# Performance work log

Hardware: AMD Instinct MI355X
Metric: run time of the kernel (lower is better)

## Reference

```python
import jax, jax.numpy as jnp
import numpy as np
from jax.ops import segment_sum, segment_max

N_NODES = 50000
N_GRAPHS = 64
EPS = 1e-16


def gat_layer(x, src, dst, W, a_src, a_dst, b, n_nodes):
    # PyG GATConv, heads=1: shared linear, additive attention, per-dst softmax
    h = x @ W                                  # [N, H]
    al_s = h @ a_src                           # [N]
    al_d = h @ a_dst                           # [N]
    e = jax.nn.leaky_relu(al_s[src] + al_d[dst], 0.2)   # [E]
    # numerically stable segment softmax over edges grouped by dst
    m = segment_max(e, dst, num_segments=n_nodes)
    m = jnp.where(jnp.isfinite(m), m, 0.0)
    ex = jnp.exp(e - m[dst])
    denom = segment_sum(ex, dst, num_segments=n_nodes)
    alpha = ex / (denom[dst] + EPS)            # [E]
    out = segment_sum(alpha[:, None] * h[src], dst, num_segments=n_nodes)
    return out + b


def setup_inputs() -> dict:
    key = jax.random.key(0)
    ks = jax.random.split(key, 16)
    H = 128
    x = jax.random.normal(ks[0], (N_NODES, 4), dtype=jnp.float32)
    edge_index = jax.random.randint(ks[1], (2, 800000), 0, N_NODES, dtype=jnp.int64)
    batch = jnp.sort(jax.random.randint(ks[2], (N_NODES,), 0, N_GRAPHS, dtype=jnp.int64))

    def glorot(k, shape):
        lim = np.sqrt(6.0 / (shape[0] + shape[-1]))
        return jax.random.uniform(k, shape, jnp.float32, -lim, lim)

    params = {
        'W1': glorot(ks[3], (4, H)), 'as1': glorot(ks[4], (H,)), 'ad1': glorot(ks[5], (H,)), 'b1': jnp.zeros((H,), jnp.float32),
        'W2': glorot(ks[6], (H, H)), 'as2': glorot(ks[7], (H,)), 'ad2': glorot(ks[8], (H,)), 'b2': jnp.zeros((H,), jnp.float32),
        'W3': glorot(ks[9], (H, H)), 'as3': glorot(ks[10], (H,)), 'ad3': glorot(ks[11], (H,)), 'b3': jnp.zeros((H,), jnp.float32),
        'Wlin': glorot(ks[12], (H, 2)), 'blin': jnp.zeros((2,), jnp.float32),
    }
    return {'x': x, 'edge_index': edge_index, 'batch': batch, **params}


def reference(x, edge_index, batch, W1, as1, ad1, b1, W2, as2, ad2, b2, W3, as3, ad3, b3, Wlin, blin):
    n = x.shape[0]
    # GATConv default add_self_loops=True
    loop = jnp.arange(n, dtype=edge_index.dtype)
    src = jnp.concatenate([edge_index[0], loop])
    dst = jnp.concatenate([edge_index[1], loop])

    h = jax.nn.relu(gat_layer(x, src, dst, W1, as1, ad1, b1, n))
    h = jax.nn.relu(gat_layer(h, src, dst, W2, as2, ad2, b2, n))
    h = gat_layer(h, src, dst, W3, as3, ad3, b3, n)

    # global_mean_pool
    sums = segment_sum(h, batch, num_segments=N_GRAPHS)          # [G, H]
    cnt = segment_sum(jnp.ones((n,), h.dtype), batch, num_segments=N_GRAPHS)
    pooled = sums / jnp.maximum(cnt, 1.0)[:, None]
    # dropout p=0.5 is identity in eval mode
    return pooled @ Wlin + blin                                   # [G, 2]
```

## Files before the change

kernel.cpp:

```cpp
#include <hip/hip_runtime.h>
#include <math.h>


#define BW 512
#define PART_CHUNK 4096
#define HIST_WGS 256

typedef __attribute__((ext_vector_type(8))) short short8v;
typedef __attribute__((ext_vector_type(4))) float f32x4;
typedef __attribute__((ext_vector_type(4))) unsigned uint4v;

__device__ __forceinline__ float bflo(unsigned u) { return __uint_as_float(u << 16); }
__device__ __forceinline__ float bfhi(unsigned u) { return __uint_as_float(u & 0xffff0000u); }
__device__ __forceinline__ unsigned pk2bf(float a, float b) {
  unsigned ua = __float_as_uint(a); ua += 0x7fffu + ((ua >> 16) & 1u);
  unsigned ub = __float_as_uint(b); ub += 0x7fffu + ((ub >> 16) & 1u);
  return (ua >> 16) | (ub & 0xffff0000u);
}

__global__ __launch_bounds__(256) void kb_hist(const int* __restrict__ ei,
                                               int* __restrict__ bpart,
                                               int E, int ET) {
  __shared__ int h[128];
  int tid = threadIdx.x;
  if (tid < 128) h[tid] = 0;
  __syncthreads();
  int stride = HIST_WGS * 256;
  for (int i = blockIdx.x * 256 + tid; i < ET; i += stride) {
    int dst = (i < E) ? ei[E + i] : (i - E);
    atomicAdd(&h[dst >> 9], 1);
  }
  __syncthreads();
  if (tid < 128) bpart[blockIdx.x * 128 + tid] = h[tid];
}

__global__ __launch_bounds__(128) void kb_scan(const int* __restrict__ bpart,
                                               int* __restrict__ bbase,
                                               int* __restrict__ bcur,
                                               int* __restrict__ rowp,
                                               int N, int ET, int NB) {
  __shared__ int sm[128];
  int t = threadIdx.x;
  int v = 0;
  for (int w = 0; w < HIST_WGS; ++w) v += bpart[w * 128 + t];
  if (t >= NB) v = 0;
  sm[t] = v;
  __syncthreads();
  for (int off = 1; off < 128; off <<= 1) {
    int u = (t >= off) ? sm[t - off] : 0;
    __syncthreads();
    sm[t] += u;
    __syncthreads();
  }
  int pre = sm[t] - v;
  if (t <= NB) bbase[t] = pre;
  if (t < NB) bcur[t] = pre;
  if (t == 0) rowp[N] = ET;
}

__global__ __launch_bounds__(256) void kb_part(const int* __restrict__ ei,
                                               int* __restrict__ bcur,
                                               int* __restrict__ bucketed,
                                               int E, int ET, int NB) {
  __shared__ int hist[128];
  __shared__ int runb[128];
  int tid = threadIdx.x;
  int base = blockIdx.x * PART_CHUNK;
  if (tid < 128) hist[tid] = 0;

  int sv[16], dv[16];
#pragma unroll
  for (int k = 0; k < 16; ++k) {
    int j = base + k * 256 + tid;
    int s = -1, d = 0;
    if (j < ET) {
      if (j < E) { s = ei[j]; d = ei[E + j]; }
      else       { s = j - E; d = j - E; }
    }
    sv[k] = s; dv[k] = d;
  }
  __syncthreads();
#pragma unroll
  for (int k = 0; k < 16; ++k)
    if (sv[k] >= 0) atomicAdd(&hist[dv[k] >> 9], 1);
  __syncthreads();
  if (tid < NB && hist[tid] > 0) runb[tid] = atomicAdd(&bcur[tid], hist[tid]);
  __syncthreads();
  if (tid < 128) hist[tid] = 0;
  __syncthreads();
#pragma unroll
  for (int k = 0; k < 16; ++k) {
    if (sv[k] >= 0) {
      int b = dv[k] >> 9;
      int off = atomicAdd(&hist[b], 1);
      bucketed[runb[b] + off] = (sv[k] << 9) | (dv[k] & (BW - 1));
    }
  }
}

__global__ __launch_bounds__(256) void kb_csr(const int* __restrict__ bucketed,
                                              const int* __restrict__ bbase,
                                              int* __restrict__ rowp,
                                              int* __restrict__ csr,
                                              int N) {
  __shared__ int h[512];
  __shared__ int sm[256];
  __shared__ int cur[512];
  int tid = threadIdx.x;
  int b = blockIdx.x;
  int cb = bbase[b], ce = bbase[b + 1];

  h[tid] = 0; h[tid + 256] = 0;
  __syncthreads();
  for (int j = cb + tid; j < ce; j += 256)
    atomicAdd(&h[bucketed[j] & (BW - 1)], 1);
  __syncthreads();
  int a0 = h[2 * tid], a1 = h[2 * tid + 1];
  int s = a0 + a1;
  sm[tid] = s;
  __syncthreads();
  for (int off = 1; off < 256; off <<= 1) {
    int u = (tid >= off) ? sm[tid - off] : 0;
    __syncthreads();
    sm[tid] += u;
    __syncthreads();
  }
  int pre = sm[tid] - s;
  cur[2 * tid] = pre;
  cur[2 * tid + 1] = pre + a0;
  __syncthreads();
  int node0 = b * BW;
  for (int local = tid; local < BW; local += 256) {
    int node = node0 + local;
    if (node < N) rowp[node] = cb + cur[local];
  }
  __syncthreads();
  for (int j = cb + tid; j < ce; j += 256) {
    int p = bucketed[j];
    int loc = p & (BW - 1);
    int pos = cb + atomicAdd(&cur[loc], 1);
    csr[pos] = (unsigned)p >> 9;
  }
}

__global__ __launch_bounds__(256) void k_prep(const float* __restrict__ W2,
                                              const float* __restrict__ W3,
                                              const float* __restrict__ W1,
                                              const float* __restrict__ as1,
                                              const float* __restrict__ ad1,
                                              unsigned short* __restrict__ Wcm2,
                                              unsigned short* __restrict__ Wcm3,
                                              float* __restrict__ wv,
                                              float* __restrict__ gsum) {
  if (blockIdx.x >= 65) {
    int idx = (blockIdx.x - 65) * 256 + threadIdx.x;
    if (idx < 64 * 128 + 64) gsum[idx] = 0.f;
    return;
  }
  if (blockIdx.x == 64) {
    int lane = threadIdx.x;
    if (lane >= 64) return;
    float2 a = *(const float2*)(as1 + lane * 2);
    float2 d = *(const float2*)(ad1 + lane * 2);
    float ps[4], pd[4];
#pragma unroll
    for (int k = 0; k < 4; ++k) {
      float2 w = *(const float2*)(W1 + k * 128 + lane * 2);
      ps[k] = w.x * a.x + w.y * a.y;
      pd[k] = w.x * d.x + w.y * d.y;
    }
    for (int off = 32; off; off >>= 1) {
#pragma unroll
      for (int k = 0; k < 4; ++k) {
        ps[k] += __shfl_xor(ps[k], off);
        pd[k] += __shfl_xor(pd[k], off);
      }
    }
    if (lane == 0) {
#pragma unroll
      for (int k = 0; k < 4; ++k) { wv[k] = ps[k]; wv[4 + k] = pd[k]; }
    }
    return;
  }
  int i = blockIdx.x * 256 + threadIdx.x;
  if (i < 16384) {
    int k = i >> 7, n = i & 127;
    unsigned u = __float_as_uint(W2[i]); u += 0x7fffu + ((u >> 16) & 1u);
    Wcm2[n * 128 + k] = (unsigned short)(u >> 16);
    unsigned v = __float_as_uint(W3[i]); v += 0x7fffu + ((v >> 16) & 1u);
    Wcm3[n * 128 + k] = (unsigned short)(v >> 16);
  }
}

__global__ __launch_bounds__(256) void k_aggx1(const int* __restrict__ csr_src,
                                               const int* __restrict__ rowp,
                                               const float* __restrict__ wv,
                                               const float* __restrict__ X,
                                               const float* __restrict__ W,
                                               const float* __restrict__ bias,
                                               float* __restrict__ exw,
                                               unsigned* __restrict__ Ybf, int N) {
  int wid = threadIdx.x >> 6, lane = threadIdx.x & 63;
  int dst = blockIdx.x * 4 + wid;
  if (dst >= N) return;
  int beg = rowp[dst], end = rowp[dst + 1];
  int deg = end - beg;
  float wvs0 = wv[0], wvs1 = wv[1], wvs2 = wv[2], wvs3 = wv[3];
  float4 xd = *(const float4*)(X + (size_t)dst * 4);
  float ald = xd.x * wv[4] + xd.y * wv[5] + xd.z * wv[6] + xd.w * wv[7];
  float4 acc = {0.f, 0.f, 0.f, 0.f};

  if (deg <= 64) {
    int srcv = 0;
    float e = -INFINITY;
    float4 xv = {0.f, 0.f, 0.f, 0.f};
    if (lane < deg) {
      srcv = csr_src[beg + lane];
      xv = *(const float4*)(X + (size_t)srcv * 4);
      float als = xv.x * wvs0 + xv.y * wvs1 + xv.z * wvs2 + xv.w * wvs3;
      e = als + ald;
      e = (e > 0.f) ? e : 0.2f * e;
    }
    float m = e;
    for (int off = 32; off; off >>= 1) m = fmaxf(m, __shfl_xor(m, off));
    float av = (lane < deg) ? __expf(e - m) : 0.f;
    float den = av;
    for (int off = 32; off; off >>= 1) den += __shfl_xor(den, off);
    av *= 1.0f / (den + 1e-16f);
    acc.x = av * xv.x; acc.y = av * xv.y; acc.z = av * xv.z; acc.w = av * xv.w;
  } else {
    float m = -INFINITY;
    for (int j = beg + lane; j < end; j += 64) {
      int s = csr_src[j];
      float4 xv = *(const float4*)(X + (size_t)s * 4);
      float e = xv.x * wvs0 + xv.y * wvs1 + xv.z * wvs2 + xv.w * wvs3 + ald;
      e = (e > 0.f) ? e : 0.2f * e;
      exw[j] = e;
      m = fmaxf(m, e);
    }
    for (int off = 32; off; off >>= 1) m = fmaxf(m, __shfl_xor(m, off));
    float den = 0.f;
    for (int j = beg + lane; j < end; j += 64) {
      float ex = __expf(exw[j] - m);
      exw[j] = ex;
      den += ex;
    }
    for (int off = 32; off; off >>= 1) den += __shfl_xor(den, off);
    float inv = 1.0f / (den + 1e-16f);
    for (int j = beg + lane; j < end; j += 64) {
      int s = csr_src[j];
      float w = exw[j] * inv;
      float4 xv = *(const float4*)(X + (size_t)s * 4);
      acc.x += w * xv.x; acc.y += w * xv.y; acc.z += w * xv.z; acc.w += w * xv.w;
    }
  }
  for (int off = 32; off; off >>= 1) {
    acc.x += __shfl_xor(acc.x, off);
    acc.y += __shfl_xor(acc.y, off);
    acc.z += __shfl_xor(acc.z, off);
    acc.w += __shfl_xor(acc.w, off);
  }
  int f = lane * 2;
  float2 w0 = *(const float2*)(W + f);
  float2 w1 = *(const float2*)(W + 128 + f);
  float2 w2 = *(const float2*)(W + 256 + f);
  float2 w3 = *(const float2*)(W + 384 + f);
  float2 bv = *(const float2*)(bias + f);
  float h0 = acc.x * w0.x + acc.y * w1.x + acc.z * w2.x + acc.w * w3.x + bv.x;
  float h1 = acc.x * w0.y + acc.y * w1.y + acc.z * w2.y + acc.w * w3.y + bv.y;
  h0 = fmaxf(h0, 0.f); h1 = fmaxf(h1, 0.f);
  __builtin_nontemporal_store(pk2bf(h0, h1), Ybf + (size_t)dst * 64 + lane);
}

__global__ __launch_bounds__(256) void k_gemm128mfma(
    const unsigned short* __restrict__ Xbf,
    const unsigned short* __restrict__ Wcm,
    const float* __restrict__ asv, const float* __restrict__ adv,
    unsigned* __restrict__ Hbf,
    float* __restrict__ al_s, float* __restrict__ al_d, int N) {
  int wid = threadIdx.x >> 6, lane = threadIdx.x & 63;
  int c = lane & 15, g = lane >> 4;
  int row0 = blockIdx.x * 64 + wid * 16;
  int arow = row0 + c;
  int arowc = (arow < N) ? arow : (N - 1);

  short8v a[4];
#pragma unroll
  for (int kt = 0; kt < 4; ++kt)
    a[kt] = *(const short8v*)(Xbf + (size_t)arowc * 128 + kt * 32 + g * 8);

  f32x4 acc[8];
#pragma unroll
  for (int f = 0; f < 8; ++f) acc[f] = (f32x4){0.f, 0.f, 0.f, 0.f};

#pragma unroll
  for (int f = 0; f < 8; ++f) {
    const unsigned short* wb = Wcm + (size_t)(f * 16 + c) * 128 + g * 8;
#pragma unroll
    for (int kt = 0; kt < 4; ++kt) {
      short8v b = *(const short8v*)(wb + kt * 32);
      acc[f] = __builtin_amdgcn_mfma_f32_16x16x32_bf16(a[kt], b, acc[f], 0, 0, 0);
    }
  }

  float ps[4] = {0.f, 0.f, 0.f, 0.f}, pd[4] = {0.f, 0.f, 0.f, 0.f};
#pragma unroll
  for (int f = 0; f < 8; ++f) {
    float as_c = asv[f * 16 + c], ad_c = adv[f * 16 + c];
#pragma unroll
    for (int j = 0; j < 4; ++j) { ps[j] += acc[f][j] * as_c; pd[j] += acc[f][j] * ad_c; }
  }
#pragma unroll
  for (int j = 0; j < 4; ++j) {
    for (int off = 1; off < 16; off <<= 1) {
      ps[j] += __shfl_xor(ps[j], off);
      pd[j] += __shfl_xor(pd[j], off);
    }
  }
  if (c == 0) {
#pragma unroll
    for (int j = 0; j < 4; ++j) {
      int r = row0 + g * 4 + j;
      if (r < N) { al_s[r] = ps[j]; al_d[r] = pd[j]; }
    }
  }

#pragma unroll
  for (int f = 0; f < 8; ++f) {
#pragma unroll
    for (int j = 0; j < 4; ++j) {
      float partner = __shfl_xor(acc[f][j], 1);
      int r = row0 + g * 4 + j;
      if (((lane & 1) == 0) && r < N)
        __builtin_nontemporal_store(pk2bf(acc[f][j], partner),
                                    Hbf + (size_t)r * 64 + f * 8 + (c >> 1));
    }
  }
}

__global__ __launch_bounds__(256) void k_agg(const int* __restrict__ csr_src,
                                             const int* __restrict__ rowp,
                                             const float* __restrict__ al_s,
                                             const float* __restrict__ al_d,
                                             const uint4* __restrict__ Hbf,
                                             const float* __restrict__ bias,
                                             float* __restrict__ exw,
                                             unsigned* __restrict__ Ybf,
                                             int N, int relu) {
  int wid = threadIdx.x >> 6, lane = threadIdx.x & 63;
  int dst = blockIdx.x * 4 + wid;
  if (dst >= N) return;
  int beg = rowp[dst], end = rowp[dst + 1];
  int deg = end - beg;
  float ald = al_d[dst];

  int q = lane >> 4;
  int l = lane & 15;
  float acc[8];
#pragma unroll
  for (int c = 0; c < 8; ++c) acc[c] = 0.f;

  if (deg <= 64) {
    int srcv = 0;
    float e = -INFINITY;
    if (lane < deg) {
      srcv = csr_src[beg + lane];
      e = al_s[srcv] + ald;
      e = (e > 0.f) ? e : 0.2f * e;
    }
    float m = e;
    for (int off = 32; off; off >>= 1) m = fmaxf(m, __shfl_xor(m, off));
    float av = (lane < deg) ? __expf(e - m) : 0.f;
    float den = av;
    for (int off = 32; off; off >>= 1) den += __shfl_xor(den, off);
    av *= 1.0f / (den + 1e-16f);

    int t = 0;
    for (; t + 16 <= deg; t += 16) {
      int s0 = __shfl(srcv, t + q);
      int s1 = __shfl(srcv, t + 4 + q);
      int s2 = __shfl(srcv, t + 8 + q);
      int s3 = __shfl(srcv, t + 12 + q);
      float w0 = __shfl(av, t + q);
      float w1 = __shfl(av, t + 4 + q);
      float w2 = __shfl(av, t + 8 + q);
      float w3 = __shfl(av, t + 12 + q);
      uint4 v0 = Hbf[(size_t)s0 * 16 + l];
      uint4 v1 = Hbf[(size_t)s1 * 16 + l];
      uint4 v2 = Hbf[(size_t)s2 * 16 + l];
      uint4 v3 = Hbf[(size_t)s3 * 16 + l];
      acc[0] += w0 * bflo(v0.x) + w1 * bflo(v1.x) + w2 * bflo(v2.x) + w3 * bflo(v3.x);
      acc[1] += w0 * bfhi(v0.x) + w1 * bfhi(v1.x) + w2 * bfhi(v2.x) + w3 * bfhi(v3.x);
      acc[2] += w0 * bflo(v0.y) + w1 * bflo(v1.y) + w2 * bflo(v2.y) + w3 * bflo(v3.y);
      acc[3] += w0 * bfhi(v0.y) + w1 * bfhi(v1.y) + w2 * bfhi(v2.y) + w3 * bfhi(v3.y);
      acc[4] += w0 * bflo(v0.z) + w1 * bflo(v1.z) + w2 * bflo(v2.z) + w3 * bflo(v3.z);
      acc[5] += w0 * bfhi(v0.z) + w1 * bfhi(v1.z) + w2 * bfhi(v2.z) + w3 * bfhi(v3.z);
      acc[6] += w0 * bflo(v0.w) + w1 * bflo(v1.w) + w2 * bflo(v2.w) + w3 * bflo(v3.w);
      acc[7] += w0 * bfhi(v0.w) + w1 * bfhi(v1.w) + w2 * bfhi(v2.w) + w3 * bfhi(v3.w);
    }
    if (t + 8 <= deg) {
      int sA = __shfl(srcv, t + q);
      int sB = __shfl(srcv, t + 4 + q);
      float wA = __shfl(av, t + q);
      float wB = __shfl(av, t + 4 + q);
      uint4 va = Hbf[(size_t)sA * 16 + l];
      uint4 vb = Hbf[(size_t)sB * 16 + l];
      acc[0] += wA * bflo(va.x) + wB * bflo(vb.x);
      acc[1] += wA * bfhi(va.x) + wB * bfhi(vb.x);
      acc[2] += wA * bflo(va.y) + wB * bflo(vb.y);
      acc[3] += wA * bfhi(va.y) + wB * bfhi(vb.y);
      acc[4] += wA * bflo(va.z) + wB * bflo(vb.z);
      acc[5] += wA * bfhi(va.z) + wB * bfhi(vb.z);
      acc[6] += wA * bflo(va.w) + wB * bflo(vb.w);
      acc[7] += wA * bfhi(va.w) + wB * bfhi(vb.w);
      t += 8;
    }
    if (t + 4 <= deg) {
      int sA = __shfl(srcv, t + q);
      float wA = __shfl(av, t + q);
      uint4 va = Hbf[(size_t)sA * 16 + l];
      acc[0] += wA * bflo(va.x); acc[1] += wA * bfhi(va.x);
      acc[2] += wA * bflo(va.y); acc[3] += wA * bfhi(va.y);
      acc[4] += wA * bflo(va.z); acc[5] += wA * bfhi(va.z);
      acc[6] += wA * bflo(va.w); acc[7] += wA * bfhi(va.w);
      t += 4;
    }
    {
      int sA = __shfl(srcv, t + q);
      float wA = __shfl(av, t + q);
      if (t + q < deg) {
        uint4 va = Hbf[(size_t)sA * 16 + l];
        acc[0] += wA * bflo(va.x); acc[1] += wA * bfhi(va.x);
        acc[2] += wA * bflo(va.y); acc[3] += wA * bfhi(va.y);
        acc[4] += wA * bflo(va.z); acc[5] += wA * bfhi(va.z);
        acc[6] += wA * bflo(va.w); acc[7] += wA * bfhi(va.w);
      }
    }
  } else {
    float m = -INFINITY;
    for (int j = beg + lane; j < end; j += 64) {
      float e = al_s[csr_src[j]] + ald;
      e = (e > 0.f) ? e : 0.2f * e;
      exw[j] = e;
      m = fmaxf(m, e);
    }
    for (int off = 32; off; off >>= 1) m = fmaxf(m, __shfl_xor(m, off));

    float den = 0.f;
    for (int j = beg + lane; j < end; j += 64) {
      float ex = __expf(exw[j] - m);
      exw[j] = ex;
      den += ex;
    }
    for (int off = 32; off; off >>= 1) den += __shfl_xor(den, off);
    float inv = 1.0f / (den + 1e-16f);

    for (int j = beg + q; j < end; j += 4) {
      int sA = csr_src[j];
      float wA = exw[j] * inv;
      uint4 va = Hbf[(size_t)sA * 16 + l];
      acc[0] += wA * bflo(va.x); acc[1] += wA * bfhi(va.x);
      acc[2] += wA * bflo(va.y); acc[3] += wA * bfhi(va.y);
      acc[4] += wA * bflo(va.z); acc[5] += wA * bfhi(va.z);
      acc[6] += wA * bflo(va.w); acc[7] += wA * bfhi(va.w);
    }
  }

#pragma unroll
  for (int c = 0; c < 8; ++c) {
    acc[c] += __shfl_xor(acc[c], 16);
    acc[c] += __shfl_xor(acc[c], 32);
  }
  if (q == 0) {
    float4 bv0 = *(const float4*)(bias + l * 8);
    float4 bv1 = *(const float4*)(bias + l * 8 + 4);
    float o0 = acc[0] + bv0.x, o1 = acc[1] + bv0.y, o2 = acc[2] + bv0.z, o3 = acc[3] + bv0.w;
    float o4 = acc[4] + bv1.x, o5 = acc[5] + bv1.y, o6 = acc[6] + bv1.z, o7 = acc[7] + bv1.w;
    if (relu) {
      o0 = fmaxf(o0, 0.f); o1 = fmaxf(o1, 0.f); o2 = fmaxf(o2, 0.f); o3 = fmaxf(o3, 0.f);
      o4 = fmaxf(o4, 0.f); o5 = fmaxf(o5, 0.f); o6 = fmaxf(o6, 0.f); o7 = fmaxf(o7, 0.f);
    }
    uint4v pb;
    pb.x = pk2bf(o0, o1); pb.y = pk2bf(o2, o3);
    pb.z = pk2bf(o4, o5); pb.w = pk2bf(o6, o7);
    __builtin_nontemporal_store(pb, (uint4v*)(Ybf + (size_t)dst * 64 + l * 4));
  }
}

__global__ __launch_bounds__(256) void k_pool(const unsigned* __restrict__ Ybf,
                                              const int* __restrict__ batch,
                                              float* __restrict__ gsum,
                                              float* __restrict__ gcnt,
                                              int N, int nwaves) {
  int gw = (blockIdx.x * 256 + threadIdx.x) >> 6;
  int lane = threadIdx.x & 63;
  int chunk = (N + nwaves - 1) / nwaves;
  int beg = gw * chunk;
  int end = beg + chunk; if (end > N) end = N;
  if (beg >= end) return;

  int curg = batch[beg];
  float2 acc = {0.f, 0.f};
  int cnt = 0;
  for (int n = beg; n < end; ++n) {
    int g = batch[n];
    if (g != curg) {
      atomicAdd(&gsum[curg * 128 + lane * 2], acc.x);
      atomicAdd(&gsum[curg * 128 + lane * 2 + 1], acc.y);
      if (lane == 0) atomicAdd(&gcnt[curg], (float)cnt);
      acc.x = 0.f; acc.y = 0.f; cnt = 0; curg = g;
    }
    unsigned u = Ybf[(size_t)n * 64 + lane];
    acc.x += bflo(u); acc.y += bfhi(u);
    ++cnt;
  }
  atomicAdd(&gsum[curg * 128 + lane * 2], acc.x);
  atomicAdd(&gsum[curg * 128 + lane * 2 + 1], acc.y);
  if (lane == 0) atomicAdd(&gcnt[curg], (float)cnt);
}

__global__ __launch_bounds__(128) void k_final(const float* __restrict__ gsum,
                                               const float* __restrict__ gcnt,
                                               const float* __restrict__ Wlin,
                                               const float* __restrict__ blin,
                                               float* __restrict__ out) {
  int t = threadIdx.x;
  int g = t >> 1, c = t & 1;
  float inv = 1.0f / fmaxf(gcnt[g], 1.0f);
  float acc = blin[c];
  for (int k = 0; k < 128; ++k) acc += gsum[g * 128 + k] * inv * Wlin[k * 2 + c];
  out[g * 2 + c] = acc;
}

extern "C" void kernel_launch(void* const* d_in, const int* in_sizes, int n_in,
                              void* d_out, int out_size, void* d_ws, size_t ws_size,
                              hipStream_t stream) {
  const float* x    = (const float*)d_in[0];
  const int*   ei   = (const int*)d_in[1];
  const int*   batch= (const int*)d_in[2];
  const float* W1   = (const float*)d_in[3];
  const float* as1  = (const float*)d_in[4];
  const float* ad1  = (const float*)d_in[5];
  const float* b1   = (const float*)d_in[6];
  const float* W2   = (const float*)d_in[7];
  const float* as2  = (const float*)d_in[8];
  const float* ad2  = (const float*)d_in[9];
  const float* b2   = (const float*)d_in[10];
  const float* W3   = (const float*)d_in[11];
  const float* as3  = (const float*)d_in[12];
  const float* ad3  = (const float*)d_in[13];
  const float* b3   = (const float*)d_in[14];
  const float* Wlin = (const float*)d_in[15];
  const float* blin = (const float*)d_in[16];

  int N = in_sizes[0] / 4;
  int E = in_sizes[1] / 2;
  int ET = E + N;
  int NB = (N + BW - 1) / BW;

  char* ws = (char*)d_ws;
  unsigned* bfA = (unsigned*)ws; ws += (size_t)N * 64 * 4;
  unsigned* bfB = (unsigned*)ws; ws += (size_t)N * 64 * 4;
  float* al_s = (float*)ws; ws += (size_t)N * 4;
  float* al_d = (float*)ws; ws += (size_t)N * 4;
  float* wv   = (float*)ws; ws += (size_t)64 * 4;
  float* gsum = (float*)ws; ws += (size_t)64 * 128 * 4;
  float* gcnt = (float*)ws; ws += (size_t)64 * 4;
  int* rowp   = (int*)ws;   ws += (size_t)(N + 1) * 4;
  int* csr    = (int*)ws;   ws += (size_t)ET * 4;
  float* exw  = (float*)ws; ws += (size_t)ET * 4;
  int* bucketed = (int*)ws; ws += (size_t)ET * 4;
  int* bpart  = (int*)ws;   ws += (size_t)HIST_WGS * 128 * 4;
  int* bbase  = (int*)ws;   ws += (size_t)132 * 4;
  int* bcur   = (int*)ws;   ws += (size_t)128 * 4;
  unsigned short* wcm2 = (unsigned short*)ws; ws += (size_t)128 * 128 * 2;
  unsigned short* wcm3 = (unsigned short*)ws; ws += (size_t)128 * 128 * 2;

  kb_hist<<<HIST_WGS, 256, 0, stream>>>(ei, bpart, E, ET);
  kb_scan<<<1, 128, 0, stream>>>(bpart, bbase, bcur, rowp, N, ET, NB);
  kb_part<<<(ET + PART_CHUNK - 1) / PART_CHUNK, 256, 0, stream>>>(ei, bcur, bucketed, E, ET, NB);
  kb_csr <<<NB, 256, 0, stream>>>(bucketed, bbase, rowp, csr, N);
  k_prep <<<98, 256, 0, stream>>>(W2, W3, W1, as1, ad1, wcm2, wcm3, wv, gsum);

  int nb4 = (N + 3) / 4;
  int nb64 = (N + 63) / 64;
  k_aggx1<<<nb4, 256, 0, stream>>>(csr, rowp, wv, x, W1, b1, exw, bfB, N);
  k_gemm128mfma<<<nb64, 256, 0, stream>>>((const unsigned short*)bfB, wcm2, as2, ad2, bfA, al_s, al_d, N);
  k_agg        <<<nb4, 256, 0, stream>>>(csr, rowp, al_s, al_d, (const uint4*)bfA, b2, exw, bfB, N, 1);
  k_gemm128mfma<<<nb64, 256, 0, stream>>>((const unsigned short*)bfB, wcm3, as3, ad3, bfA, al_s, al_d, N);
  k_agg        <<<nb4, 256, 0, stream>>>(csr, rowp, al_s, al_d, (const uint4*)bfA, b3, exw, bfB, N, 0);

  k_pool <<<256, 256, 0, stream>>>(bfB, batch, gsum, gcnt, N, 1024);
  k_final<<<1, 128, 0, stream>>>(gsum, gcnt, Wlin, blin, (float*)d_out);
}
```

Before: 312.5 us.

## Process two destination nodes per wavefront in aggregation kernels and merge CSR/prep launches

```diff
diff --git a/kernel.cpp b/kernel.cpp
--- a/kernel.cpp
+++ b/kernel.cpp
@@ -4,11 +4,12 @@
 
 #define BW 512
 #define PART_CHUNK 4096
-#define HIST_WGS 256
+#define HIST_WGS 64
 
 typedef __attribute__((ext_vector_type(8))) short short8v;
 typedef __attribute__((ext_vector_type(4))) float f32x4;
 typedef __attribute__((ext_vector_type(4))) unsigned uint4v;
+typedef __attribute__((ext_vector_type(2))) unsigned uint2v;
 
 __device__ __forceinline__ float bflo(unsigned u) { return __uint_as_float(u << 16); }
 __device__ __forceinline__ float bfhi(unsigned u) { return __uint_as_float(u & 0xffff0000u); }
@@ -98,15 +99,65 @@
   }
 }
 
-__global__ __launch_bounds__(256) void kb_csr(const int* __restrict__ bucketed,
-                                              const int* __restrict__ bbase,
-                                              int* __restrict__ rowp,
-                                              int* __restrict__ csr,
-                                              int N) {
+__global__ __launch_bounds__(256) void kb_csrprep(const int* __restrict__ bucketed,
+                                                  const int* __restrict__ bbase,
+                                                  int* __restrict__ rowp,
+                                                  int* __restrict__ csr,
+                                                  const float* __restrict__ W2,
+                                                  const float* __restrict__ W3,
+                                                  const float* __restrict__ W1,
+                                                  const float* __restrict__ as1,
+                                                  const float* __restrict__ ad1,
+                                                  unsigned short* __restrict__ Wcm2,
+                                                  unsigned short* __restrict__ Wcm3,
+                                                  float* __restrict__ wv,
+                                                  float* __restrict__ gsum,
+                                                  int N, int NB) {
+  int tid = threadIdx.x;
+  if ((int)blockIdx.x >= NB) {
+    int pb = blockIdx.x - NB;
+    if (pb >= 65) {
+      int idx = (pb - 65) * 256 + tid;
+      if (idx < 64 * 128 + 64) gsum[idx] = 0.f;
+      return;
+    }
+    if (pb == 64) {
+      if (tid >= 64) return;
+      float2 a = *(const float2*)(as1 + tid * 2);
+      float2 d = *(const float2*)(ad1 + tid * 2);
+      float ps[4], pd[4];
+#pragma unroll
+      for (int k = 0; k < 4; ++k) {
+        float2 w = *(const float2*)(W1 + k * 128 + tid * 2);
+        ps[k] = w.x * a.x + w.y * a.y;
+        pd[k] = w.x * d.x + w.y * d.y;
+      }
+      for (int off = 32; off; off >>= 1) {
+#pragma unroll
+        for (int k = 0; k < 4; ++k) {
+          ps[k] += __shfl_xor(ps[k], off);
+          pd[k] += __shfl_xor(pd[k], off);
+        }
+      }
+      if (tid == 0) {
+#pragma unroll
+        for (int k = 0; k < 4; ++k) { wv[k] = ps[k]; wv[4 + k] = pd[k]; }
+      }
+      return;
+    }
+    int i = pb * 256 + tid;
+    if (i < 16384) {
+      int k = i >> 7, n = i & 127;
+      unsigned u = __float_as_uint(W2[i]); u += 0x7fffu + ((u >> 16) & 1u);
+      Wcm2[n * 128 + k] = (unsigned short)(u >> 16);
+      unsigned v = __float_as_uint(W3[i]); v += 0x7fffu + ((v >> 16) & 1u);
+      Wcm3[n * 128 + k] = (unsigned short)(v >> 16);
+    }
+    return;
+  }
   __shared__ int h[512];
   __shared__ int sm[256];
   __shared__ int cur[512];
-  int tid = threadIdx.x;
   int b = blockIdx.x;
   int cb = bbase[b], ce = bbase[b + 1];
 
@@ -143,73 +194,96 @@
   }
 }
 
-__global__ __launch_bounds__(256) void k_prep(const float* __restrict__ W2,
-                                              const float* __restrict__ W3,
-                                              const float* __restrict__ W1,
-                                              const float* __restrict__ as1,
-                                              const float* __restrict__ ad1,
-                                              unsigned short* __restrict__ Wcm2,
-                                              unsigned short* __restrict__ Wcm3,
-                                              float* __restrict__ wv,
-                                              float* __restrict__ gsum) {
-  if (blockIdx.x >= 65) {
-    int idx = (blockIdx.x - 65) * 256 + threadIdx.x;
-    if (idx < 64 * 128 + 64) gsum[idx] = 0.f;
-    return;
-  }
-  if (blockIdx.x == 64) {
-    int lane = threadIdx.x;
-    if (lane >= 64) return;
-    float2 a = *(const float2*)(as1 + lane * 2);
-    float2 d = *(const float2*)(ad1 + lane * 2);
-    float ps[4], pd[4];
-#pragma unroll
-    for (int k = 0; k < 4; ++k) {
-      float2 w = *(const float2*)(W1 + k * 128 + lane * 2);
-      ps[k] = w.x * a.x + w.y * a.y;
-      pd[k] = w.x * d.x + w.y * d.y;
-    }
-    for (int off = 32; off; off >>= 1) {
-#pragma unroll
-      for (int k = 0; k < 4; ++k) {
-        ps[k] += __shfl_xor(ps[k], off);
-        pd[k] += __shfl_xor(pd[k], off);
-      }
-    }
-    if (lane == 0) {
-#pragma unroll
-      for (int k = 0; k < 4; ++k) { wv[k] = ps[k]; wv[4 + k] = pd[k]; }
-    }
-    return;
-  }
-  int i = blockIdx.x * 256 + threadIdx.x;
-  if (i < 16384) {
-    int k = i >> 7, n = i & 127;
-    unsigned u = __float_as_uint(W2[i]); u += 0x7fffu + ((u >> 16) & 1u);
-    Wcm2[n * 128 + k] = (unsigned short)(u >> 16);
-    unsigned v = __float_as_uint(W3[i]); v += 0x7fffu + ((v >> 16) & 1u);
-    Wcm3[n * 128 + k] = (unsigned short)(v >> 16);
-  }
-}
-
-__global__ __launch_bounds__(256) void k_aggx1(const int* __restrict__ csr_src,
-                                               const int* __restrict__ rowp,
-                                               const float* __restrict__ wv,
-                                               const float* __restrict__ X,
-                                               const float* __restrict__ W,
-                                               const float* __restrict__ bias,
-                                               float* __restrict__ exw,
-                                               unsigned* __restrict__ Ybf, int N) {
-  int wid = threadIdx.x >> 6, lane = threadIdx.x & 63;
-  int dst = blockIdx.x * 4 + wid;
-  if (dst >= N) return;
-  int beg = rowp[dst], end = rowp[dst + 1];
+__device__ __forceinline__ void agg_full64(int beg, int end, float ald, int dst,
+    const int* __restrict__ csr_src, const float* __restrict__ al_s,
+    const uint4* __restrict__ Hbf, const float* __restrict__ bias,
+    float* __restrict__ exw, unsigned* __restrict__ Ybf, int relu) {
+  int lane = threadIdx.x & 63;
   int deg = end - beg;
-  float wvs0 = wv[0], wvs1 = wv[1], wvs2 = wv[2], wvs3 = wv[3];
-  float4 xd = *(const float4*)(X + (size_t)dst * 4);
-  float ald = xd.x * wv[4] + xd.y * wv[5] + xd.z * wv[6] + xd.w * wv[7];
+  int q = lane >> 4, l = lane & 15;
+  float acc[8];
+#pragma unroll
+  for (int c = 0; c < 8; ++c) acc[c] = 0.f;
+
+  if (deg <= 64) {
+    int srcv = 0;
+    float e = -INFINITY;
+    if (lane < deg) {
+      srcv = csr_src[beg + lane];
+      e = al_s[srcv] + ald;
+      e = (e > 0.f) ? e : 0.2f * e;
+    }
+    float m = e;
+    for (int off = 32; off; off >>= 1) m = fmaxf(m, __shfl_xor(m, off));
+    float av = (lane < deg) ? __expf(e - m) : 0.f;
+    float den = av;
+    for (int off = 32; off; off >>= 1) den += __shfl_xor(den, off);
+    av *= 1.0f / (den + 1e-16f);
+    for (int t = 0; t < deg; t += 4) {
+      int sA = __shfl(srcv, t + q);
+      float wA = __shfl(av, t + q);
+      uint4 va = Hbf[(size_t)sA * 16 + l];
+      acc[0] += wA * bflo(va.x); acc[1] += wA * bfhi(va.x);
+      acc[2] += wA * bflo(va.y); acc[3] += wA * bfhi(va.y);
+      acc[4] += wA * bflo(va.z); acc[5] += wA * bfhi(va.z);
+      acc[6] += wA * bflo(va.w); acc[7] += wA * bfhi(va.w);
+    }
+  } else {
+    float m = -INFINITY;
+    for (int j = beg + lane; j < end; j += 64) {
+      float e = al_s[csr_src[j]] + ald;
+      e = (e > 0.f) ? e : 0.2f * e;
+      exw[j] = e;
+      m = fmaxf(m, e);
+    }
+    for (int off = 32; off; off >>= 1) m = fmaxf(m, __shfl_xor(m, off));
+    float den = 0.f;
+    for (int j = beg + lane; j < end; j += 64) {
+      float ex = __expf(exw[j] - m);
+      exw[j] = ex;
+      den += ex;
+    }
+    for (int off = 32; off; off >>= 1) den += __shfl_xor(den, off);
+    float inv = 1.0f / (den + 1e-16f);
+    for (int j = beg + q; j < end; j += 4) {
+      int sA = csr_src[j];
+      float wA = exw[j] * inv;
+      uint4 va = Hbf[(size_t)sA * 16 + l];
+      acc[0] += wA * bflo(va.x); acc[1] += wA * bfhi(va.x);
+      acc[2] += wA * bflo(va.y); acc[3] += wA * bfhi(va.y);
+      acc[4] += wA * bflo(va.z); acc[5] += wA * bfhi(va.z);
+      acc[6] += wA * bflo(va.w); acc[7] += wA * bfhi(va.w);
+    }
+  }
+#pragma unroll
+  for (int c = 0; c < 8; ++c) {
+    acc[c] += __shfl_xor(acc[c], 16);
+    acc[c] += __shfl_xor(acc[c], 32);
+  }
+  if (q == 0) {
+    float4 bv0 = *(const float4*)(bias + l * 8);
+    float4 bv1 = *(const float4*)(bias + l * 8 + 4);
+    float o0 = acc[0] + bv0.x, o1 = acc[1] + bv0.y, o2 = acc[2] + bv0.z, o3 = acc[3] + bv0.w;
+    float o4 = acc[4] + bv1.x, o5 = acc[5] + bv1.y, o6 = acc[6] + bv1.z, o7 = acc[7] + bv1.w;
+    if (relu) {
+      o0 = fmaxf(o0, 0.f); o1 = fmaxf(o1, 0.f); o2 = fmaxf(o2, 0.f); o3 = fmaxf(o3, 0.f);
+      o4 = fmaxf(o4, 0.f); o5 = fmaxf(o5, 0.f); o6 = fmaxf(o6, 0.f); o7 = fmaxf(o7, 0.f);
+    }
+    uint4v pb;
+    pb.x = pk2bf(o0, o1); pb.y = pk2bf(o2, o3);
+    pb.z = pk2bf(o4, o5); pb.w = pk2bf(o6, o7);
+    __builtin_nontemporal_store(pb, (uint4v*)(Ybf + (size_t)dst * 64 + l * 4));
+  }
+}
+
+__device__ __forceinline__ void aggx1_full64(int beg, int end, float ald, int dst,
+    const int* __restrict__ csr_src, const float* __restrict__ X,
+    float wvs0, float wvs1, float wvs2, float wvs3,
+    const float* __restrict__ W, const float* __restrict__ bias,
+    float* __restrict__ exw, unsigned* __restrict__ Ybf) {
+  int lane = threadIdx.x & 63;
+  int deg = end - beg;
   float4 acc = {0.f, 0.f, 0.f, 0.f};
-
   if (deg <= 64) {
     int srcv = 0;
     float e = -INFINITY;
@@ -217,8 +291,7 @@
     if (lane < deg) {
       srcv = csr_src[beg + lane];
       xv = *(const float4*)(X + (size_t)srcv * 4);
-      float als = xv.x * wvs0 + xv.y * wvs1 + xv.z * wvs2 + xv.w * wvs3;
-      e = als + ald;
+      e = xv.x * wvs0 + xv.y * wvs1 + xv.z * wvs2 + xv.w * wvs3 + ald;
       e = (e > 0.f) ? e : 0.2f * e;
     }
     float m = e;
@@ -272,6 +345,88 @@
   __builtin_nontemporal_store(pk2bf(h0, h1), Ybf + (size_t)dst * 64 + lane);
 }
 
+__global__ __launch_bounds__(256) void k_aggx1(const int* __restrict__ csr_src,
+                                               const int* __restrict__ rowp,
+                                               const float* __restrict__ wv,
+                                               const float* __restrict__ X,
+                                               const float* __restrict__ W,
+                                               const float* __restrict__ bias,
+                                               float* __restrict__ exw,
+                                               unsigned* __restrict__ Ybf, int N) {
+  int wid = threadIdx.x >> 6, lane = threadIdx.x & 63;
+  int half = lane >> 5, il = lane & 31;
+  int d0 = blockIdx.x * 8 + wid * 2;
+  if (d0 >= N) return;
+  float wvs0 = wv[0], wvs1 = wv[1], wvs2 = wv[2], wvs3 = wv[3];
+  float wvd0 = wv[4], wvd1 = wv[5], wvd2 = wv[6], wvd3 = wv[7];
+
+  int dst = d0 + half;
+  bool vdst = dst < N;
+  int beg = 0, end = 0;
+  if (vdst) { beg = rowp[dst]; end = rowp[dst + 1]; }
+  int deg = end - beg;
+  int mx = max(deg, __shfl_xor(deg, 32));
+
+  float ald = 0.f;
+  if (vdst) {
+    float4 xd = *(const float4*)(X + (size_t)dst * 4);
+    ald = xd.x * wvd0 + xd.y * wvd1 + xd.z * wvd2 + xd.w * wvd3;
+  }
+
+  if (mx <= 32) {
+    int srcv = 0;
+    float e = -INFINITY;
+    float4 xv = {0.f, 0.f, 0.f, 0.f};
+    if (il < deg) {
+      srcv = csr_src[beg + il];
+      xv = *(const float4*)(X + (size_t)srcv * 4);
+      float e0 = xv.x * wvs0 + xv.y * wvs1 + xv.z * wvs2 + xv.w * wvs3 + ald;
+      e = (e0 > 0.f) ? e0 : 0.2f * e0;
+    }
+    float m = e;
+    for (int off = 16; off; off >>= 1) m = fmaxf(m, __shfl_xor(m, off));
+    float av = (il < deg) ? __expf(e - m) : 0.f;
+    float den = av;
+    for (int off = 16; off; off >>= 1) den += __shfl_xor(den, off);
+    av *= 1.0f / (den + 1e-16f);
+    float4 acc;
+    acc.x = av * xv.x; acc.y = av * xv.y; acc.z = av * xv.z; acc.w = av * xv.w;
+    for (int off = 16; off; off >>= 1) {
+      acc.x += __shfl_xor(acc.x, off);
+      acc.y += __shfl_xor(acc.y, off);
+      acc.z += __shfl_xor(acc.z, off);
+      acc.w += __shfl_xor(acc.w, off);
+    }
+    int f = il * 4;
+    float4 w0 = *(const float4*)(W + f);
+    float4 w1 = *(const float4*)(W + 128 + f);
+    float4 w2 = *(const float4*)(W + 256 + f);
+    float4 w3 = *(const float4*)(W + 384 + f);
+    float4 bv = *(const float4*)(bias + f);
+    float h0 = acc.x * w0.x + acc.y * w1.x + acc.z * w2.x + acc.w * w3.x + bv.x;
+    float h1 = acc.x * w0.y + acc.y * w1.y + acc.z * w2.y + acc.w * w3.y + bv.y;
+    float h2 = acc.x * w0.z + acc.y * w1.z + acc.z * w2.z + acc.w * w3.z + bv.z;
+    float h3 = acc.x * w0.w + acc.y * w1.w + acc.z * w2.w + acc.w * w3.w + bv.w;
+    h0 = fmaxf(h0, 0.f); h1 = fmaxf(h1, 0.f);
+    h2 = fmaxf(h2, 0.f); h3 = fmaxf(h3, 0.f);
+    if (vdst) {
+      uint2v pb;
+      pb.x = pk2bf(h0, h1); pb.y = pk2bf(h2, h3);
+      __builtin_nontemporal_store(pb, (uint2v*)(Ybf + (size_t)dst * 64 + il * 2));
+    }
+  } else {
+    for (int k = 0; k < 2; ++k) {
+      int d = d0 + k;
+      if (d < N) {
+        int b = rowp[d], en = rowp[d + 1];
+        float4 xd = *(const float4*)(X + (size_t)d * 4);
+        float a2 = xd.x * wvd0 + xd.y * wvd1 + xd.z * wvd2 + xd.w * wvd3;
+        aggx1_full64(b, en, a2, d, csr_src, X, wvs0, wvs1, wvs2, wvs3, W, bias, exw, Ybf);
+      }
+    }
+  }
+}
+
 __global__ __launch_bounds__(256) void k_gemm128mfma(
     const unsigned short* __restrict__ Xbf,
     const unsigned short* __restrict__ Wcm,
@@ -348,43 +503,47 @@
                                              unsigned* __restrict__ Ybf,
                                              int N, int relu) {
   int wid = threadIdx.x >> 6, lane = threadIdx.x & 63;
-  int dst = blockIdx.x * 4 + wid;
-  if (dst >= N) return;
-  int beg = rowp[dst], end = rowp[dst + 1];
+  int half = lane >> 5, il = lane & 31;
+  int d0 = blockIdx.x * 8 + wid * 2;
+  if (d0 >= N) return;
+  int dst = d0 + half;
+  bool vdst = dst < N;
+  int beg = 0, end = 0;
+  if (vdst) { beg = rowp[dst]; end = rowp[dst + 1]; }
   int deg = end - beg;
-  float ald = al_d[dst];
-
-  int q = lane >> 4;
-  int l = lane & 15;
-  float acc[8];
-#pragma unroll
-  for (int c = 0; c < 8; ++c) acc[c] = 0.f;
-
-  if (deg <= 64) {
+  int mx = max(deg, __shfl_xor(deg, 32));
+  float ald = vdst ? al_d[dst] : 0.f;
+
+  if (mx <= 32) {
     int srcv = 0;
     float e = -INFINITY;
-    if (lane < deg) {
-      srcv = csr_src[beg + lane];
+    if (il < deg) {
+      srcv = csr_src[beg + il];
       e = al_s[srcv] + ald;
       e = (e > 0.f) ? e : 0.2f * e;
     }
     float m = e;
-    for (int off = 32; off; off >>= 1) m = fmaxf(m, __shfl_xor(m, off));
-    float av = (lane < deg) ? __expf(e - m) : 0.f;
+    for (int off = 16; off; off >>= 1) m = fmaxf(m, __shfl_xor(m, off));
+    float av = (il < deg) ? __expf(e - m) : 0.f;
     float den = av;
-    for (int off = 32; off; off >>= 1) den += __shfl_xor(den, off);
+    for (int off = 16; off; off >>= 1) den += __shfl_xor(den, off);
     av *= 1.0f / (den + 1e-16f);
 
-    int t = 0;
-    for (; t + 16 <= deg; t += 16) {
-      int s0 = __shfl(srcv, t + q);
-      int s1 = __shfl(srcv, t + 4 + q);
-      int s2 = __shfl(srcv, t + 8 + q);
-      int s3 = __shfl(srcv, t + 12 + q);
-      float w0 = __shfl(av, t + q);
-      float w1 = __shfl(av, t + 4 + q);
-      float w2 = __shfl(av, t + 8 + q);
-      float w3 = __shfl(av, t + 12 + q);
+    int q = il >> 4, l = il & 15;
+    int b32 = lane & 32;
+    float acc[8];
+#pragma unroll
+    for (int c = 0; c < 8; ++c) acc[c] = 0.f;
+
+    for (int t = 0; t < mx; t += 8) {
+      int s0 = __shfl(srcv, b32 + t + q);
+      int s1 = __shfl(srcv, b32 + t + 2 + q);
+      int s2 = __shfl(srcv, b32 + t + 4 + q);
+      int s3 = __shfl(srcv, b32 + t + 6 + q);
+      float w0 = __shfl(av, b32 + t + q);
+      float w1 = __shfl(av, b32 + t + 2 + q);
+      float w2 = __shfl(av, b32 + t + 4 + q);
+      float w3 = __shfl(av, b32 + t + 6 + q);
       uint4 v0 = Hbf[(size_t)s0 * 16 + l];
       uint4 v1 = Hbf[(size_t)s1 * 16 + l];
       uint4 v2 = Hbf[(size_t)s2 * 16 + l];
@@ -398,92 +557,30 @@
       acc[6] += w0 * bflo(v0.w) + w1 * bflo(v1.w) + w2 * bflo(v2.w) + w3 * bflo(v3.w);
       acc[7] += w0 * bfhi(v0.w) + w1 * bfhi(v1.w) + w2 * bfhi(v2.w) + w3 * bfhi(v3.w);
     }
-    if (t + 8 <= deg) {
-      int sA = __shfl(srcv, t + q);
-      int sB = __shfl(srcv, t + 4 + q);
-      float wA = __shfl(av, t + q);
-      float wB = __shfl(av, t + 4 + q);
-      uint4 va = Hbf[(size_t)sA * 16 + l];
-      uint4 vb = Hbf[(size_t)sB * 16 + l];
-      acc[0] += wA * bflo(va.x) + wB * bflo(vb.x);
-      acc[1] += wA * bfhi(va.x) + wB * bfhi(vb.x);
-      acc[2] += wA * bflo(va.y) + wB * bflo(vb.y);
-      acc[3] += wA * bfhi(va.y) + wB * bfhi(vb.y);
-      acc[4] += wA * bflo(va.z) + wB * bflo(vb.z);
-      acc[5] += wA * bfhi(va.z) + wB * bfhi(vb.z);
-      acc[6] += wA * bflo(va.w) + wB * bflo(vb.w);
-      acc[7] += wA * bfhi(va.w) + wB * bfhi(vb.w);
-      t += 8;
-    }
-    if (t + 4 <= deg) {
-      int sA = __shfl(srcv, t + q);
-      float wA = __shfl(av, t + q);
-      uint4 va = Hbf[(size_t)sA * 16 + l];
-      acc[0] += wA * bflo(va.x); acc[1] += wA * bfhi(va.x);
-      acc[2] += wA * bflo(va.y); acc[3] += wA * bfhi(va.y);
-      acc[4] += wA * bflo(va.z); acc[5] += wA * bfhi(va.z);
-      acc[6] += wA * bflo(va.w); acc[7] += wA * bfhi(va.w);
-      t += 4;
-    }
-    {
-      int sA = __shfl(srcv, t + q);
-      float wA = __shfl(av, t + q);
-      if (t + q < deg) {
-        uint4 va = Hbf[(size_t)sA * 16 + l];
-        acc[0] += wA * bflo(va.x); acc[1] += wA * bfhi(va.x);
-        acc[2] += wA * bflo(va.y); acc[3] += wA * bfhi(va.y);
-        acc[4] += wA * bflo(va.z); acc[5] += wA * bfhi(va.z);
-        acc[6] += wA * bflo(va.w); acc[7] += wA * bfhi(va.w);
+#pragma unroll
+    for (int c = 0; c < 8; ++c) acc[c] += __shfl_xor(acc[c], 16);
+    if (q == 0 && vdst) {
+      float4 bv0 = *(const float4*)(bias + l * 8);
+      float4 bv1 = *(const float4*)(bias + l * 8 + 4);
+      float o0 = acc[0] + bv0.x, o1 = acc[1] + bv0.y, o2 = acc[2] + bv0.z, o3 = acc[3] + bv0.w;
+      float o4 = acc[4] + bv1.x, o5 = acc[5] + bv1.y, o6 = acc[6] + bv1.z, o7 = acc[7] + bv1.w;
+      if (relu) {
+        o0 = fmaxf(o0, 0.f); o1 = fmaxf(o1, 0.f); o2 = fmaxf(o2, 0.f); o3 = fmaxf(o3, 0.f);
+        o4 = fmaxf(o4, 0.f); o5 = fmaxf(o5, 0.f); o6 = fmaxf(o6, 0.f); o7 = fmaxf(o7, 0.f);
       }
+      uint4v pb;
+      pb.x = pk2bf(o0, o1); pb.y = pk2bf(o2, o3);
+      pb.z = pk2bf(o4, o5); pb.w = pk2bf(o6, o7);
+      __builtin_nontemporal_store(pb, (uint4v*)(Ybf + (size_t)dst * 64 + l * 4));
     }
   } else {
-    float m = -INFINITY;
-    for (int j = beg + lane; j < end; j += 64) {
-      float e = al_s[csr_src[j]] + ald;
-      e = (e > 0.f) ? e : 0.2f * e;
-      exw[j] = e;
-      m = fmaxf(m, e);
-    }
-    for (int off = 32; off; off >>= 1) m = fmaxf(m, __shfl_xor(m, off));
-
-    float den = 0.f;
-    for (int j = beg + lane; j < end; j += 64) {
-      float ex = __expf(exw[j] - m);
-      exw[j] = ex;
-      den += ex;
-    }
-    for (int off = 32; off; off >>= 1) den += __shfl_xor(den, off);
-    float inv = 1.0f / (den + 1e-16f);
-
-    for (int j = beg + q; j < end; j += 4) {
-      int sA = csr_src[j];
-      float wA = exw[j] * inv;
-      uint4 va = Hbf[(size_t)sA * 16 + l];
-      acc[0] += wA * bflo(va.x); acc[1] += wA * bfhi(va.x);
-      acc[2] += wA * bflo(va.y); acc[3] += wA * bfhi(va.y);
-      acc[4] += wA * bflo(va.z); acc[5] += wA * bfhi(va.z);
-      acc[6] += wA * bflo(va.w); acc[7] += wA * bfhi(va.w);
-    }
-  }
-
-#pragma unroll
-  for (int c = 0; c < 8; ++c) {
-    acc[c] += __shfl_xor(acc[c], 16);
-    acc[c] += __shfl_xor(acc[c], 32);
-  }
-  if (q == 0) {
-    float4 bv0 = *(const float4*)(bias + l * 8);
-    float4 bv1 = *(const float4*)(bias + l * 8 + 4);
-    float o0 = acc[0] + bv0.x, o1 = acc[1] + bv0.y, o2 = acc[2] + bv0.z, o3 = acc[3] + bv0.w;
-    float o4 = acc[4] + bv1.x, o5 = acc[5] + bv1.y, o6 = acc[6] + bv1.z, o7 = acc[7] + bv1.w;
-    if (relu) {
-      o0 = fmaxf(o0, 0.f); o1 = fmaxf(o1, 0.f); o2 = fmaxf(o2, 0.f); o3 = fmaxf(o3, 0.f);
-      o4 = fmaxf(o4, 0.f); o5 = fmaxf(o5, 0.f); o6 = fmaxf(o6, 0.f); o7 = fmaxf(o7, 0.f);
-    }
-    uint4v pb;
-    pb.x = pk2bf(o0, o1); pb.y = pk2bf(o2, o3);
-    pb.z = pk2bf(o4, o5); pb.w = pk2bf(o6, o7);
-    __builtin_nontemporal_store(pb, (uint4v*)(Ybf + (size_t)dst * 64 + l * 4));
+    for (int k = 0; k < 2; ++k) {
+      int d = d0 + k;
+      if (d < N) {
+        int b = rowp[d], en = rowp[d + 1];
+        agg_full64(b, en, al_d[d], d, csr_src, al_s, Hbf, bias, exw, Ybf, relu);
+      }
+    }
   }
 }
 
@@ -579,16 +676,16 @@
   kb_hist<<<HIST_WGS, 256, 0, stream>>>(ei, bpart, E, ET);
   kb_scan<<<1, 128, 0, stream>>>(bpart, bbase, bcur, rowp, N, ET, NB);
   kb_part<<<(ET + PART_CHUNK - 1) / PART_CHUNK, 256, 0, stream>>>(ei, bcur, bucketed, E, ET, NB);
-  kb_csr <<<NB, 256, 0, stream>>>(bucketed, bbase, rowp, csr, N);
-  k_prep <<<98, 256, 0, stream>>>(W2, W3, W1, as1, ad1, wcm2, wcm3, wv, gsum);
-
-  int nb4 = (N + 3) / 4;
+  kb_csrprep<<<NB + 98, 256, 0, stream>>>(bucketed, bbase, rowp, csr,
+                                          W2, W3, W1, as1, ad1, wcm2, wcm3, wv, gsum, N, NB);
+
+  int nb8 = (N + 7) / 8;
   int nb64 = (N + 63) / 64;
-  k_aggx1<<<nb4, 256, 0, stream>>>(csr, rowp, wv, x, W1, b1, exw, bfB, N);
+  k_aggx1<<<nb8, 256, 0, stream>>>(csr, rowp, wv, x, W1, b1, exw, bfB, N);
   k_gemm128mfma<<<nb64, 256, 0, stream>>>((const unsigned short*)bfB, wcm2, as2, ad2, bfA, al_s, al_d, N);
-  k_agg        <<<nb4, 256, 0, stream>>>(csr, rowp, al_s, al_d, (const uint4*)bfA, b2, exw, bfB, N, 1);
+  k_agg        <<<nb8, 256, 0, stream>>>(csr, rowp, al_s, al_d, (const uint4*)bfA, b2, exw, bfB, N, 1);
   k_gemm128mfma<<<nb64, 256, 0, stream>>>((const unsigned short*)bfB, wcm3, as3, ad3, bfA, al_s, al_d, N);
-  k_agg        <<<nb4, 256, 0, stream>>>(csr, rowp, al_s, al_d, (const uint4*)bfA, b3, exw, bfB, N, 0);
+  k_agg        <<<nb8, 256, 0, stream>>>(csr, rowp, al_s, al_d, (const uint4*)bfA, b3, exw, bfB, N, 0);
 
   k_pool <<<256, 256, 0, stream>>>(bfB, batch, gsum, gcnt, N, 1024);
   k_final<<<1, 128, 0, stream>>>(gsum, gcnt, Wlin, blin, (float*)d_out);
```

Result: no change. 308.0 us (-1.5%).
